# Optimization experiments

Measured on AMD Instinct MI355X. Metric: run time of the kernel, lower is better.

Reference implementation:

```python
import jax, jax.numpy as jnp
import numpy as np

B, LQ, LKV, D = 16, 2048, 2048, 64

def setup_inputs() -> dict:
    key = jax.random.key(0)
    k1, k2, k3 = jax.random.split(key, 3)
    return {
        "query": jax.random.normal(k1, (B, LQ, D), dtype=jnp.float32),
        "key": jax.random.normal(k2, (B, LKV, D), dtype=jnp.float32),
        "value": jax.random.normal(k3, (B, LKV, D), dtype=jnp.float32),
        "scale_factor": 8,   # sqrt(D)
        "dropout_p": 0,      # identity dropout (original p=1 zeros output; degenerate)
    }

def reference(query, key, value, scale_factor, dropout_p):
    # qk: [B, LQ, LKV]
    scores = jnp.einsum("bqd,bkd->bqk", query, key) / scale_factor
    probs = jax.nn.softmax(scores, axis=-1)
    # dropout_p == 0 -> dropout is the identity
    out = jnp.einsum("bqk,bkd->bqd", probs, value)
    return out
```

## Files before the change

kernel.cpp:

```cpp
#include <hip/hip_runtime.h>
#include <hip/hip_bf16.h>
#include <cstdint>

#define BATCH 16
#define LQ    2048
#define LKV   2048
#define DH    64
#define QT    64
#define KT    64
#define WAVES 4
#define LOG2E 1.4426950408889634f

typedef __attribute__((ext_vector_type(4))) float  f32x4;
typedef __attribute__((ext_vector_type(8))) __bf16 bf16x8;
typedef __attribute__((ext_vector_type(4))) __bf16 bf16x4;

#define OFF_K 0
#define OFF_V 8192
#define PS    72
#define OFF_P 16384
#define SMEM_MAIN (OFF_P + WAVES * 16 * PS * 2)

#define GLL16(gp, lp) __builtin_amdgcn_global_load_lds( \
    (const __attribute__((address_space(1))) uint32_t*)(gp), \
    (__attribute__((address_space(3))) uint32_t*)(lp), 16, 0, 0)

__device__ __forceinline__ float read_scale(const int* scale_p) {
    int iv = scale_p[0];
    if (iv > (1 << 23)) { union { int i; float f; } u; u.i = iv; return u.f; }
    return (float)iv;
}

__global__ __launch_bounds__(256) void preconv(
    const float* __restrict__ Kg, const float* __restrict__ Vg,
    __bf16* __restrict__ Kb, __bf16* __restrict__ Vt)
{
    __shared__ __bf16 sT[64 * 72];
    const int tid = threadIdx.x;
    const int b = blockIdx.x & 15;
    const int t = blockIdx.x >> 4;
    const size_t base = ((size_t)b * LKV + (size_t)t * 64) * DH;

    {
        const int r = tid >> 2, cs = (tid & 3) * 16;
        const float* gk = Kg + base + (size_t)r * DH + cs;
        f32x4 a0 = *(const f32x4*)(gk + 0);
        f32x4 a1 = *(const f32x4*)(gk + 4);
        f32x4 a2 = *(const f32x4*)(gk + 8);
        f32x4 a3 = *(const f32x4*)(gk + 12);
        float f[16];
        *(f32x4*)&f[0] = a0; *(f32x4*)&f[4] = a1;
        *(f32x4*)&f[8] = a2; *(f32x4*)&f[12] = a3;
        bf16x8 w0, w1;
        for (int i = 0; i < 8; ++i) { w0[i] = (__bf16)f[i]; w1[i] = (__bf16)f[i + 8]; }
        __bf16* dst = Kb + base + (size_t)r * DH + cs;
        *(bf16x8*)dst = w0; *(bf16x8*)(dst + 8) = w1;
    }
    {
        const int vd0 = (tid & 15) * 4, vk0 = (tid >> 4) * 4;
        const float* gv = Vg + base + (size_t)vk0 * DH + vd0;
        f32x4 vr[4];
        for (int j = 0; j < 4; ++j) vr[j] = *(const f32x4*)(gv + (size_t)j * DH);
        for (int i = 0; i < 4; ++i) {
            bf16x4 w;
            w[0] = (__bf16)vr[0][i]; w[1] = (__bf16)vr[1][i];
            w[2] = (__bf16)vr[2][i]; w[3] = (__bf16)vr[3][i];
            *(bf16x4*)(&sT[(vd0 + i) * 72 + vk0]) = w;
        }
    }
    __syncthreads();
    {
        const int d = tid >> 2, ks = (tid & 3) * 16;
        bf16x8 w0 = *(const bf16x8*)(&sT[d * 72 + ks]);
        bf16x8 w1 = *(const bf16x8*)(&sT[d * 72 + ks + 8]);
        __bf16* dst = Vt + ((size_t)b * DH + d) * LKV + (size_t)t * 64 + ks;
        *(bf16x8*)dst = w0; *(bf16x8*)(dst + 8) = w1;
    }
}

template<int SPLITS>
__global__ __launch_bounds__(256, 4) void attn_main(
    const float* __restrict__ Qg, const __bf16* __restrict__ Kb,
    const __bf16* __restrict__ Vt, const int* __restrict__ scale_p,
    float* __restrict__ Og, float* __restrict__ Lg)
{
    __shared__ __align__(16) char smem[SMEM_MAIN];
    char*   sK = smem + OFF_K;
    char*   sV = smem + OFF_V;
    __bf16* sP = (__bf16*)(smem + OFF_P);

    const int tid  = threadIdx.x;
    const int lane = tid & 63;
    const int wave = tid >> 6;
    const int g    = lane >> 4;
    const int n    = lane & 15;

    const int b     = blockIdx.x & 15;
    const int t2    = blockIdx.x >> 4;
    const int split = (SPLITS == 1) ? 0 : (t2 % SPLITS);
    const int qt    = (SPLITS == 1) ? t2 : (t2 / SPLITS);
    const int q0    = qt * QT;
    const int NTS   = LKV / (KT * SPLITS);
    const int kvbase = split * (LKV / SPLITS);

    const float sc = (1.0f / read_scale(scale_p)) * LOG2E;

    bf16x8 qhi[2], qlo[2];
    {
        const float* qr = Qg + ((size_t)b * LQ + q0 + wave * 16 + n) * DH;
        for (int h = 0; h < 2; ++h) {
            const float* src = qr + h * 32 + g * 8;
            f32x4 x = *(const f32x4*)(src);
            f32x4 y = *(const f32x4*)(src + 4);
            float f[8];
            *(f32x4*)&f[0] = x; *(f32x4*)&f[4] = y;
            bf16x8 h8, l8;
            for (int i = 0; i < 8; ++i) {
                __bf16 hb = (__bf16)f[i];
                h8[i] = hb;
                l8[i] = (__bf16)(f[i] - (float)hb);
            }
            qhi[h] = h8; qlo[h] = l8;
        }
    }

    const int fOA = n * 128 + (((0 + g) ^ (n & 7)) << 4);
    const int fOB = n * 128 + (((4 + g) ^ (n & 7)) << 4);
    char* pwW = (char*)sP + wave * (16 * PS * 2) + n * (PS * 2) + g * 8;
    char* pwR = (char*)sP + wave * (16 * PS * 2) + n * (PS * 2) + g * 16;

    const int r8  = lane >> 3;
    const int sgi = (lane & 7) ^ r8;
    const char* kg0 = (const char*)(Kb + ((size_t)b * LKV + kvbase + wave * 16 + r8) * DH) + sgi * 16;
    const char* kg1 = kg0 + 8 * DH * 2;
    const char* vg0 = (const char*)(Vt + ((size_t)b * DH + wave * 16 + r8) * LKV + kvbase) + sgi * 16;
    const char* vg1 = vg0 + 8 * LKV * 2;
    char* lK0 = sK + wave * 16 * 128; char* lK1 = lK0 + 1024;
    char* lV0 = sV + wave * 16 * 128; char* lV1 = lV0 + 1024;

    float lsum = 0.0f;
    f32x4 o[4];
    const f32x4 zero4 = {0.f, 0.f, 0.f, 0.f};
    for (int mc = 0; mc < 4; ++mc) o[mc] = zero4;

    for (int kt = 0; kt < NTS; ++kt) {
        __syncthreads();
        GLL16(kg0, lK0); GLL16(kg1, lK1);
        GLL16(vg0, lV0); GLL16(vg1, lV1);
        kg0 += KT * DH * 2; kg1 += KT * DH * 2;
        vg0 += KT * 2;      vg1 += KT * 2;
        __syncthreads();

        f32x4 s[4];
        for (int c = 0; c < 4; ++c) s[c] = zero4;
        for (int c = 0; c < 4; ++c) {
            bf16x8 kf0 = *(const bf16x8*)(sK + c * 2048 + fOA);
            bf16x8 kf1 = *(const bf16x8*)(sK + c * 2048 + fOB);
            s[c] = __builtin_amdgcn_mfma_f32_16x16x32_bf16(kf0, qhi[0], s[c], 0, 0, 0);
            s[c] = __builtin_amdgcn_mfma_f32_16x16x32_bf16(kf0, qlo[0], s[c], 0, 0, 0);
            s[c] = __builtin_amdgcn_mfma_f32_16x16x32_bf16(kf1, qhi[1], s[c], 0, 0, 0);
            s[c] = __builtin_amdgcn_mfma_f32_16x16x32_bf16(kf1, qlo[1], s[c], 0, 0, 0);
        }

        for (int c = 0; c < 4; ++c) {
            float p0 = __builtin_amdgcn_exp2f(s[c][0] * sc);
            float p1 = __builtin_amdgcn_exp2f(s[c][1] * sc);
            float p2 = __builtin_amdgcn_exp2f(s[c][2] * sc);
            float p3 = __builtin_amdgcn_exp2f(s[c][3] * sc);
            lsum += (p0 + p1) + (p2 + p3);
            bf16x4 w;
            w[0] = (__bf16)p0; w[1] = (__bf16)p1; w[2] = (__bf16)p2; w[3] = (__bf16)p3;
            *(bf16x4*)(pwW + c * 32) = w;
        }
        __asm__ volatile("s_waitcnt lgkmcnt(0)" ::: "memory");

        bf16x8 pb0 = *(const bf16x8*)(pwR);
        bf16x8 pb1 = *(const bf16x8*)(pwR + 64);

        for (int mc = 0; mc < 4; ++mc) {
            bf16x8 vf0 = *(const bf16x8*)(sV + mc * 2048 + fOA);
            bf16x8 vf1 = *(const bf16x8*)(sV + mc * 2048 + fOB);
            o[mc] = __builtin_amdgcn_mfma_f32_16x16x32_bf16(vf0, pb0, o[mc], 0, 0, 0);
            o[mc] = __builtin_amdgcn_mfma_f32_16x16x32_bf16(vf1, pb1, o[mc], 0, 0, 0);
        }
    }

    lsum += __shfl_xor(lsum, 16, 64);
    lsum += __shfl_xor(lsum, 32, 64);

    const size_t qrow = (size_t)(q0 + wave * 16 + n);
    if (SPLITS == 1) {
        float rl = 1.0f / lsum;
        float* dst = Og + ((size_t)b * LQ + qrow) * DH + 4 * g;
        for (int mc = 0; mc < 4; ++mc) {
            f32x4 v = o[mc];
            v[0] *= rl; v[1] *= rl; v[2] *= rl; v[3] *= rl;
            *(f32x4*)(dst + mc * 16) = v;
        }
    } else {
        float* dst = Og + (((size_t)split * BATCH + b) * LQ + qrow) * DH + 4 * g;
        for (int mc = 0; mc < 4; ++mc)
            *(f32x4*)(dst + mc * 16) = o[mc];
        if (g == 0)
            Lg[((size_t)split * BATCH + b) * LQ + qrow] = lsum;
    }
}

__global__ __launch_bounds__(256) void combine2(
    const float* __restrict__ Op, const float* __restrict__ Lg,
    float* __restrict__ Og)
{
    const size_t gid = (size_t)blockIdx.x * 256 + threadIdx.x;
    const size_t row = gid >> 4;
    const int    c4  = (int)(gid & 15) * 4;
    const size_t SO  = (size_t)BATCH * LQ * DH;
    f32x4 a  = *(const f32x4*)(Op + row * DH + c4);
    f32x4 b2 = *(const f32x4*)(Op + SO + row * DH + c4);
    float rl = 1.0f / (Lg[row] + Lg[(size_t)BATCH * LQ + row]);
    f32x4 v;
    for (int i = 0; i < 4; ++i) v[i] = (a[i] + b2[i]) * rl;
    *(f32x4*)(Og + row * DH + c4) = v;
}

#define FQS 68
#define FKS 72
#define F_OFF_K 0
#define F_SZ_K  (KT * FKS * 2)
#define F_OFF_V (F_OFF_K + F_SZ_K)
#define F_SZ_V  (DH * FKS * 2)
#define F_OFF_P (F_OFF_V + F_SZ_V)
#define F_SZ_P  (WAVES * 16 * FKS * 2)
#define F_SMEM_MAIN (F_OFF_P + F_SZ_P)
#define F_SZ_Q  (QT * FQS * 4)
#define F_SMEM (F_SMEM_MAIN > F_SZ_Q ? F_SMEM_MAIN : F_SZ_Q)

__global__ __launch_bounds__(256, 2)
void attn_fallback(const float* __restrict__ Qg, const float* __restrict__ Kg,
                   const float* __restrict__ Vg, const int* __restrict__ scale_p,
                   float* __restrict__ Og)
{
    __shared__ __align__(16) char smem[F_SMEM];
    float*  sQ = (float*) (smem);
    __bf16* sK = (__bf16*)(smem + F_OFF_K);
    __bf16* sV = (__bf16*)(smem + F_OFF_V);
    __bf16* sP = (__bf16*)(smem + F_OFF_P);

    const int tid  = threadIdx.x;
    const int lane = tid & 63;
    const int wave = tid >> 6;
    const int g    = lane >> 4;
    const int n    = lane & 15;
    const int b  = blockIdx.x & 15;
    const int qt = blockIdx.x >> 4;
    const int q0 = qt * QT;
    const float scv = (1.0f / read_scale(scale_p)) * LOG2E;
    const size_t bq = (size_t)b * LQ * DH;

    {
        const int row = tid >> 2, dseg = (tid & 3) * 16;
        const float* gq = Qg + bq + (size_t)(q0 + row) * DH + dseg;
        f32x4 a0 = *(const f32x4*)(gq + 0), a1 = *(const f32x4*)(gq + 4);
        f32x4 a2 = *(const f32x4*)(gq + 8), a3 = *(const f32x4*)(gq + 12);
        f32x4* dst = (f32x4*)(sQ + row * FQS + dseg);
        dst[0] = a0; dst[1] = a1; dst[2] = a2; dst[3] = a3;
    }
    __syncthreads();

    bf16x8 qhi[2], qlo[2];
    {
        const float* qr = sQ + (wave * 16 + n) * FQS;
        for (int h = 0; h < 2; ++h) {
            const float* src = qr + h * 32 + g * 8;
            f32x4 x = *(const f32x4*)(src), y = *(const f32x4*)(src + 4);
            float f[8];
            *(f32x4*)&f[0] = x; *(f32x4*)&f[4] = y;
            bf16x8 h8, l8;
            for (int i = 0; i < 8; ++i) {
                __bf16 hb = (__bf16)f[i];
                h8[i] = hb; l8[i] = (__bf16)(f[i] - (float)hb);
            }
            qhi[h] = h8; qlo[h] = l8;
        }
    }

    float lsum = 0.0f;
    f32x4 o[4];
    const f32x4 zero4 = {0.f, 0.f, 0.f, 0.f};
    for (int mc = 0; mc < 4; ++mc) o[mc] = zero4;

    const int krow = tid >> 2, kseg = (tid & 3) * 16;
    const int vd0 = (tid & 15) * 4, vkv0 = (tid >> 4) * 4;
    const float* gK = Kg + bq + (size_t)krow * DH + kseg;
    const float* gV = Vg + bq + (size_t)vkv0 * DH + vd0;
    f32x4 kreg[4], vreg[4];
    for (int j = 0; j < 4; ++j) kreg[j] = *(const f32x4*)(gK + j * 4);
    for (int j = 0; j < 4; ++j) vreg[j] = *(const f32x4*)(gV + (size_t)j * DH);

    for (int kt = 0; kt < LKV / KT; ++kt) {
        __syncthreads();
        {
            float f[16];
            *(f32x4*)&f[0] = kreg[0]; *(f32x4*)&f[4] = kreg[1];
            *(f32x4*)&f[8] = kreg[2]; *(f32x4*)&f[12] = kreg[3];
            bf16x8 w0, w1;
            for (int i = 0; i < 8; ++i) { w0[i] = (__bf16)f[i]; w1[i] = (__bf16)f[i + 8]; }
            *(bf16x8*)(sK + krow * FKS + kseg) = w0;
            *(bf16x8*)(sK + krow * FKS + kseg + 8) = w1;
        }
        for (int i = 0; i < 4; ++i) {
            bf16x4 w;
            w[0] = (__bf16)vreg[0][i]; w[1] = (__bf16)vreg[1][i];
            w[2] = (__bf16)vreg[2][i]; w[3] = (__bf16)vreg[3][i];
            *(bf16x4*)(sV + (vd0 + i) * FKS + vkv0) = w;
        }
        __syncthreads();
        if (kt + 1 < LKV / KT) {
            const float* gK2 = gK + (size_t)(kt + 1) * KT * DH;
            const float* gV2 = gV + (size_t)(kt + 1) * KT * DH;
            for (int j = 0; j < 4; ++j) kreg[j] = *(const f32x4*)(gK2 + j * 4);
            for (int j = 0; j < 4; ++j) vreg[j] = *(const f32x4*)(gV2 + (size_t)j * DH);
        }

        f32x4 s[4];
        for (int c = 0; c < 4; ++c) s[c] = zero4;
        for (int c = 0; c < 4; ++c) {
            for (int h = 0; h < 2; ++h) {
                bf16x8 kf = *(const bf16x8*)(sK + (c * 16 + n) * FKS + h * 32 + g * 8);
                s[c] = __builtin_amdgcn_mfma_f32_16x16x32_bf16(kf, qhi[h], s[c], 0, 0, 0);
                s[c] = __builtin_amdgcn_mfma_f32_16x16x32_bf16(kf, qlo[h], s[c], 0, 0, 0);
            }
        }
        __bf16* pw = sP + wave * 16 * FKS;
        for (int c = 0; c < 4; ++c) {
            float p0 = __builtin_amdgcn_exp2f(s[c][0] * scv);
            float p1 = __builtin_amdgcn_exp2f(s[c][1] * scv);
            float p2 = __builtin_amdgcn_exp2f(s[c][2] * scv);
            float p3 = __builtin_amdgcn_exp2f(s[c][3] * scv);
            lsum += (p0 + p1) + (p2 + p3);
            bf16x4 w;
            w[0] = (__bf16)p0; w[1] = (__bf16)p1; w[2] = (__bf16)p2; w[3] = (__bf16)p3;
            *(bf16x4*)(pw + n * FKS + c * 16 + 4 * g) = w;
        }
        __asm__ volatile("s_waitcnt lgkmcnt(0)" ::: "memory");
        bf16x8 pb0 = *(const bf16x8*)(pw + n * FKS + 0  + 8 * g);
        bf16x8 pb1 = *(const bf16x8*)(pw + n * FKS + 32 + 8 * g);
        for (int mc = 0; mc < 4; ++mc) {
            bf16x8 vf0 = *(const bf16x8*)(sV + (mc * 16 + n) * FKS + 0  + 8 * g);
            bf16x8 vf1 = *(const bf16x8*)(sV + (mc * 16 + n) * FKS + 32 + 8 * g);
            o[mc] = __builtin_amdgcn_mfma_f32_16x16x32_bf16(vf0, pb0, o[mc], 0, 0, 0);
            o[mc] = __builtin_amdgcn_mfma_f32_16x16x32_bf16(vf1, pb1, o[mc], 0, 0, 0);
        }
    }
    lsum += __shfl_xor(lsum, 16, 64);
    lsum += __shfl_xor(lsum, 32, 64);
    {
        float rl = 1.0f / lsum;
        float* dst = Og + bq + (size_t)(q0 + wave * 16 + n) * DH;
        for (int mc = 0; mc < 4; ++mc) {
            f32x4 v = o[mc];
            v[0] *= rl; v[1] *= rl; v[2] *= rl; v[3] *= rl;
            *(f32x4*)(dst + mc * 16 + 4 * g) = v;
        }
    }
}

extern "C" void kernel_launch(void* const* d_in, const int* in_sizes, int n_in,
                              void* d_out, int out_size, void* d_ws, size_t ws_size,
                              hipStream_t stream)
{
    const float* Qg = (const float*)d_in[0];
    const float* Kg = (const float*)d_in[1];
    const float* Vg = (const float*)d_in[2];
    const int*   sc = (const int*)d_in[3];
    float* Og = (float*)d_out;

    const size_t szKb = (size_t)BATCH * LKV * DH * 2;
    const size_t oV   = szKb;
    const size_t oO   = 2 * szKb;
    const size_t szOp = (size_t)2 * BATCH * LQ * DH * 4;
    const size_t oL   = oO + szOp;
    const size_t need1 = oL + (size_t)2 * BATCH * LQ * 4;
    const size_t need2 = oO;

    if (ws_size >= need1) {
        __bf16* Kb = (__bf16*)d_ws;
        __bf16* Vt = (__bf16*)((char*)d_ws + oV);
        float*  Op = (float*)((char*)d_ws + oO);
        float*  Lg = (float*)((char*)d_ws + oL);
        preconv<<<dim3(BATCH * (LKV / 64)), dim3(256), 0, stream>>>(Kg, Vg, Kb, Vt);
        attn_main<2><<<dim3(BATCH * (LQ / QT) * 2), dim3(256), 0, stream>>>(Qg, Kb, Vt, sc, Op, Lg);
        combine2<<<dim3((BATCH * LQ * DH / 4) / 256), dim3(256), 0, stream>>>(Op, Lg, Og);
    } else if (ws_size >= need2) {
        __bf16* Kb = (__bf16*)d_ws;
        __bf16* Vt = (__bf16*)((char*)d_ws + oV);
        preconv<<<dim3(BATCH * (LKV / 64)), dim3(256), 0, stream>>>(Kg, Vg, Kb, Vt);
        attn_main<1><<<dim3(BATCH * (LQ / QT)), dim3(256), 0, stream>>>(Qg, Kb, Vt, sc, Og, nullptr);
    } else {
        attn_fallback<<<dim3(BATCH * (LQ / QT)), dim3(256), 0, stream>>>(Qg, Kg, Vg, sc, Og);
    }
}
```

Baseline: 112.8 us.

## Double the query tile per block and double-buffer K/V loads

```diff
diff --git a/kernel.cpp b/kernel.cpp
--- a/kernel.cpp
+++ b/kernel.cpp
@@ -6,7 +6,7 @@
 #define LQ    2048
 #define LKV   2048
 #define DH    64
-#define QT    64
+#define QT    128
 #define KT    64
 #define WAVES 4
 #define LOG2E 1.4426950408889634f
@@ -16,10 +16,10 @@
 typedef __attribute__((ext_vector_type(4))) __bf16 bf16x4;
 
 #define OFF_K 0
-#define OFF_V 8192
+#define OFF_V 16384
 #define PS    72
-#define OFF_P 16384
-#define SMEM_MAIN (OFF_P + WAVES * 16 * PS * 2)
+#define OFF_P 32768
+#define SMEM_MAIN (OFF_P + WAVES * 32 * PS * 2)
 
 #define GLL16(gp, lp) __builtin_amdgcn_global_load_lds( \
     (const __attribute__((address_space(1))) uint32_t*)(gp), \
@@ -79,15 +79,12 @@
 }
 
 template<int SPLITS>
-__global__ __launch_bounds__(256, 4) void attn_main(
+__global__ __launch_bounds__(256, 2) void attn_main(
     const float* __restrict__ Qg, const __bf16* __restrict__ Kb,
     const __bf16* __restrict__ Vt, const int* __restrict__ scale_p,
     float* __restrict__ Og, float* __restrict__ Lg)
 {
     __shared__ __align__(16) char smem[SMEM_MAIN];
-    char*   sK = smem + OFF_K;
-    char*   sV = smem + OFF_V;
-    __bf16* sP = (__bf16*)(smem + OFF_P);
 
     const int tid  = threadIdx.x;
     const int lane = tid & 63;
@@ -97,7 +94,7 @@
 
     const int b     = blockIdx.x & 15;
     const int t2    = blockIdx.x >> 4;
-    const int split = (SPLITS == 1) ? 0 : (t2 % SPLITS);
+    const int split = (SPLITS == 1) ? 0 : (t2 & (SPLITS - 1));
     const int qt    = (SPLITS == 1) ? t2 : (t2 / SPLITS);
     const int q0    = qt * QT;
     const int NTS   = LKV / (KT * SPLITS);
@@ -105,9 +102,26 @@
 
     const float sc = (1.0f / read_scale(scale_p)) * LOG2E;
 
-    bf16x8 qhi[2], qlo[2];
-    {
-        const float* qr = Qg + ((size_t)b * LQ + q0 + wave * 16 + n) * DH;
+    const int r8  = lane >> 3;
+    const int sgi = (lane & 7) ^ r8;
+    const char* kg0 = (const char*)(Kb + ((size_t)b * LKV + kvbase + wave * 16 + r8) * DH) + sgi * 16;
+    const char* kg1 = kg0 + 8 * DH * 2;
+    const char* vg0 = (const char*)(Vt + ((size_t)b * DH + wave * 16 + r8) * LKV + kvbase) + sgi * 16;
+    const char* vg1 = vg0 + 8 * LKV * 2;
+    const int kStep = KT * DH * 2;
+    const int vStep = KT * 2;
+
+    {
+        char* lK = smem + OFF_K + wave * 2048;
+        char* lV = smem + OFF_V + wave * 2048;
+        GLL16(kg0, lK); GLL16(kg1, lK + 1024);
+        GLL16(vg0, lV); GLL16(vg1, lV + 1024);
+        kg0 += kStep; kg1 += kStep; vg0 += vStep; vg1 += vStep;
+    }
+
+    bf16x8 qh[2][2], ql[2][2];
+    for (int nb = 0; nb < 2; ++nb) {
+        const float* qr = Qg + ((size_t)b * LQ + q0 + wave * 32 + nb * 16 + n) * DH;
         for (int h = 0; h < 2; ++h) {
             const float* src = qr + h * 32 + g * 8;
             f32x4 x = *(const f32x4*)(src);
@@ -120,89 +134,109 @@
                 h8[i] = hb;
                 l8[i] = (__bf16)(f[i] - (float)hb);
             }
-            qhi[h] = h8; qlo[h] = l8;
+            qh[nb][h] = h8; ql[nb][h] = l8;
         }
     }
 
     const int fOA = n * 128 + (((0 + g) ^ (n & 7)) << 4);
     const int fOB = n * 128 + (((4 + g) ^ (n & 7)) << 4);
-    char* pwW = (char*)sP + wave * (16 * PS * 2) + n * (PS * 2) + g * 8;
-    char* pwR = (char*)sP + wave * (16 * PS * 2) + n * (PS * 2) + g * 16;
-
-    const int r8  = lane >> 3;
-    const int sgi = (lane & 7) ^ r8;
-    const char* kg0 = (const char*)(Kb + ((size_t)b * LKV + kvbase + wave * 16 + r8) * DH) + sgi * 16;
-    const char* kg1 = kg0 + 8 * DH * 2;
-    const char* vg0 = (const char*)(Vt + ((size_t)b * DH + wave * 16 + r8) * LKV + kvbase) + sgi * 16;
-    const char* vg1 = vg0 + 8 * LKV * 2;
-    char* lK0 = sK + wave * 16 * 128; char* lK1 = lK0 + 1024;
-    char* lV0 = sV + wave * 16 * 128; char* lV1 = lV0 + 1024;
-
-    float lsum = 0.0f;
-    f32x4 o[4];
+    char* pwBase = smem + OFF_P + wave * (32 * PS * 2);
+    char* pwW0 = pwBase + n * (PS * 2) + g * 8;
+    char* pwR0 = pwBase + n * (PS * 2) + g * 16;
+
+    float lsum[2] = {0.0f, 0.0f};
+    f32x4 o[2][4];
     const f32x4 zero4 = {0.f, 0.f, 0.f, 0.f};
-    for (int mc = 0; mc < 4; ++mc) o[mc] = zero4;
+    for (int nb = 0; nb < 2; ++nb)
+        for (int mc = 0; mc < 4; ++mc) o[nb][mc] = zero4;
 
     for (int kt = 0; kt < NTS; ++kt) {
         __syncthreads();
-        GLL16(kg0, lK0); GLL16(kg1, lK1);
-        GLL16(vg0, lV0); GLL16(vg1, lV1);
-        kg0 += KT * DH * 2; kg1 += KT * DH * 2;
-        vg0 += KT * 2;      vg1 += KT * 2;
-        __syncthreads();
-
-        f32x4 s[4];
-        for (int c = 0; c < 4; ++c) s[c] = zero4;
+        const int cur = kt & 1;
+        char* sK = smem + OFF_K + cur * 8192;
+        char* sV = smem + OFF_V + cur * 8192;
+
+        if (kt + 1 < NTS) {
+            char* lK = smem + OFF_K + (cur ^ 1) * 8192 + wave * 2048;
+            char* lV = smem + OFF_V + (cur ^ 1) * 8192 + wave * 2048;
+            GLL16(kg0, lK); GLL16(kg1, lK + 1024);
+            GLL16(vg0, lV); GLL16(vg1, lV + 1024);
+            kg0 += kStep; kg1 += kStep; vg0 += vStep; vg1 += vStep;
+        }
+
+        f32x4 s[2][4];
+        for (int nb = 0; nb < 2; ++nb)
+            for (int c = 0; c < 4; ++c) s[nb][c] = zero4;
+        #pragma unroll
         for (int c = 0; c < 4; ++c) {
             bf16x8 kf0 = *(const bf16x8*)(sK + c * 2048 + fOA);
             bf16x8 kf1 = *(const bf16x8*)(sK + c * 2048 + fOB);
-            s[c] = __builtin_amdgcn_mfma_f32_16x16x32_bf16(kf0, qhi[0], s[c], 0, 0, 0);
-            s[c] = __builtin_amdgcn_mfma_f32_16x16x32_bf16(kf0, qlo[0], s[c], 0, 0, 0);
-            s[c] = __builtin_amdgcn_mfma_f32_16x16x32_bf16(kf1, qhi[1], s[c], 0, 0, 0);
-            s[c] = __builtin_amdgcn_mfma_f32_16x16x32_bf16(kf1, qlo[1], s[c], 0, 0, 0);
-        }
-
-        for (int c = 0; c < 4; ++c) {
-            float p0 = __builtin_amdgcn_exp2f(s[c][0] * sc);
-            float p1 = __builtin_amdgcn_exp2f(s[c][1] * sc);
-            float p2 = __builtin_amdgcn_exp2f(s[c][2] * sc);
-            float p3 = __builtin_amdgcn_exp2f(s[c][3] * sc);
-            lsum += (p0 + p1) + (p2 + p3);
-            bf16x4 w;
-            w[0] = (__bf16)p0; w[1] = (__bf16)p1; w[2] = (__bf16)p2; w[3] = (__bf16)p3;
-            *(bf16x4*)(pwW + c * 32) = w;
+            #pragma unroll
+            for (int nb = 0; nb < 2; ++nb) {
+                s[nb][c] = __builtin_amdgcn_mfma_f32_16x16x32_bf16(kf0, qh[nb][0], s[nb][c], 0, 0, 0);
+                s[nb][c] = __builtin_amdgcn_mfma_f32_16x16x32_bf16(kf0, ql[nb][0], s[nb][c], 0, 0, 0);
+                s[nb][c] = __builtin_amdgcn_mfma_f32_16x16x32_bf16(kf1, qh[nb][1], s[nb][c], 0, 0, 0);
+                s[nb][c] = __builtin_amdgcn_mfma_f32_16x16x32_bf16(kf1, ql[nb][1], s[nb][c], 0, 0, 0);
+            }
+        }
+
+        #pragma unroll
+        for (int nb = 0; nb < 2; ++nb) {
+            char* pw = pwW0 + nb * (16 * PS * 2);
+            #pragma unroll
+            for (int c = 0; c < 4; ++c) {
+                float p0 = __builtin_amdgcn_exp2f(s[nb][c][0] * sc);
+                float p1 = __builtin_amdgcn_exp2f(s[nb][c][1] * sc);
+                float p2 = __builtin_amdgcn_exp2f(s[nb][c][2] * sc);
+                float p3 = __builtin_amdgcn_exp2f(s[nb][c][3] * sc);
+                lsum[nb] += (p0 + p1) + (p2 + p3);
+                bf16x4 w;
+                w[0] = (__bf16)p0; w[1] = (__bf16)p1; w[2] = (__bf16)p2; w[3] = (__bf16)p3;
+                *(bf16x4*)(pw + c * 32) = w;
+            }
         }
         __asm__ volatile("s_waitcnt lgkmcnt(0)" ::: "memory");
 
-        bf16x8 pb0 = *(const bf16x8*)(pwR);
-        bf16x8 pb1 = *(const bf16x8*)(pwR + 64);
-
+        bf16x8 pb[2][2];
+        #pragma unroll
+        for (int nb = 0; nb < 2; ++nb) {
+            char* pr = pwR0 + nb * (16 * PS * 2);
+            pb[nb][0] = *(const bf16x8*)(pr);
+            pb[nb][1] = *(const bf16x8*)(pr + 64);
+        }
+
+        #pragma unroll
         for (int mc = 0; mc < 4; ++mc) {
             bf16x8 vf0 = *(const bf16x8*)(sV + mc * 2048 + fOA);
             bf16x8 vf1 = *(const bf16x8*)(sV + mc * 2048 + fOB);
-            o[mc] = __builtin_amdgcn_mfma_f32_16x16x32_bf16(vf0, pb0, o[mc], 0, 0, 0);
-            o[mc] = __builtin_amdgcn_mfma_f32_16x16x32_bf16(vf1, pb1, o[mc], 0, 0, 0);
-        }
-    }
-
-    lsum += __shfl_xor(lsum, 16, 64);
-    lsum += __shfl_xor(lsum, 32, 64);
-
-    const size_t qrow = (size_t)(q0 + wave * 16 + n);
-    if (SPLITS == 1) {
-        float rl = 1.0f / lsum;
-        float* dst = Og + ((size_t)b * LQ + qrow) * DH + 4 * g;
-        for (int mc = 0; mc < 4; ++mc) {
-            f32x4 v = o[mc];
-            v[0] *= rl; v[1] *= rl; v[2] *= rl; v[3] *= rl;
-            *(f32x4*)(dst + mc * 16) = v;
-        }
-    } else {
-        float* dst = Og + (((size_t)split * BATCH + b) * LQ + qrow) * DH + 4 * g;
-        for (int mc = 0; mc < 4; ++mc)
-            *(f32x4*)(dst + mc * 16) = o[mc];
-        if (g == 0)
-            Lg[((size_t)split * BATCH + b) * LQ + qrow] = lsum;
+            #pragma unroll
+            for (int nb = 0; nb < 2; ++nb) {
+                o[nb][mc] = __builtin_amdgcn_mfma_f32_16x16x32_bf16(vf0, pb[nb][0], o[nb][mc], 0, 0, 0);
+                o[nb][mc] = __builtin_amdgcn_mfma_f32_16x16x32_bf16(vf1, pb[nb][1], o[nb][mc], 0, 0, 0);
+            }
+        }
+    }
+
+    #pragma unroll
+    for (int nb = 0; nb < 2; ++nb) {
+        lsum[nb] += __shfl_xor(lsum[nb], 16, 64);
+        lsum[nb] += __shfl_xor(lsum[nb], 32, 64);
+        const size_t qrow = (size_t)(q0 + wave * 32 + nb * 16 + n);
+        if (SPLITS == 1) {
+            float rl = 1.0f / lsum[nb];
+            float* dst = Og + ((size_t)b * LQ + qrow) * DH + 4 * g;
+            for (int mc = 0; mc < 4; ++mc) {
+                f32x4 v = o[nb][mc];
+                v[0] *= rl; v[1] *= rl; v[2] *= rl; v[3] *= rl;
+                *(f32x4*)(dst + mc * 16) = v;
+            }
+        } else {
+            float* dst = Og + (((size_t)split * BATCH + b) * LQ + qrow) * DH + 4 * g;
+            for (int mc = 0; mc < 4; ++mc)
+                *(f32x4*)(dst + mc * 16) = o[nb][mc];
+            if (g == 0)
+                Lg[((size_t)split * BATCH + b) * LQ + qrow] = lsum[nb];
+        }
     }
 }
 
@@ -231,7 +265,7 @@
 #define F_OFF_P (F_OFF_V + F_SZ_V)
 #define F_SZ_P  (WAVES * 16 * FKS * 2)
 #define F_SMEM_MAIN (F_OFF_P + F_SZ_P)
-#define F_SZ_Q  (QT * FQS * 4)
+#define F_SZ_Q  (64 * FQS * 4)
 #define F_SMEM (F_SMEM_MAIN > F_SZ_Q ? F_SMEM_MAIN : F_SZ_Q)
 
 __global__ __launch_bounds__(256, 2)
@@ -252,7 +286,7 @@
     const int n    = lane & 15;
     const int b  = blockIdx.x & 15;
     const int qt = blockIdx.x >> 4;
-    const int q0 = qt * QT;
+    const int q0 = qt * 64;
     const float scv = (1.0f / read_scale(scale_p)) * LOG2E;
     const size_t bq = (size_t)b * LQ * DH;
 
@@ -396,6 +430,6 @@
         preconv<<<dim3(BATCH * (LKV / 64)), dim3(256), 0, stream>>>(Kg, Vg, Kb, Vt);
         attn_main<1><<<dim3(BATCH * (LQ / QT)), dim3(256), 0, stream>>>(Qg, Kb, Vt, sc, Og, nullptr);
     } else {
-        attn_fallback<<<dim3(BATCH * (LQ / QT)), dim3(256), 0, stream>>>(Qg, Kg, Vg, sc, Og);
-    }
-}
+        attn_fallback<<<dim3(BATCH * (LQ / 64)), dim3(256), 0, stream>>>(Qg, Kg, Vg, sc, Og);
+    }
+}
```

After: 111.9 us. Within noise of the previous version (-0.8%).
